# Kernel tuning notes

Measured on AMD Instinct MI355X. Metric: run time of the kernel, lower is better.

The kernel has to match this reference:

```python
import jax, jax.numpy as jnp
import numpy as np

B, S, D, H, M, K = 2048, 32, 1024, 1024, 4096, 32


def setup_inputs() -> dict:
    key = jax.random.key(0)
    ks = jax.random.split(key, 10)
    inp = {
        "x": jax.random.normal(ks[0], (B, S, D), dtype=jnp.float32),
        "topk": K,
        "W_enc": jax.random.normal(ks[1], (D, H), dtype=jnp.float32) * (1.0 / np.sqrt(D)),
        "b_enc": jnp.zeros((H,), dtype=jnp.float32),
        "w_curv": jax.random.normal(ks[2], (H, 1), dtype=jnp.float32) * (1.0 / np.sqrt(H)),
        "b_curv": jnp.zeros((1,), dtype=jnp.float32),
        "memory_slots": jax.random.normal(ks[3], (M, H), dtype=jnp.float32),
        "assoc": jax.random.normal(ks[4], (M, M), dtype=jnp.float32) * 0.01,
        "W_dec": jax.random.normal(ks[5], (H, D), dtype=jnp.float32) * (1.0 / np.sqrt(H)),
        "b_dec": jnp.zeros((D,), dtype=jnp.float32),
        "temperature": jnp.asarray(1.0, dtype=jnp.float32),
    }
    return inp


def reference(x, topk, W_enc, b_enc, w_curv, b_curv, memory_slots, assoc, W_dec, b_dec, temperature):
    # encoder + pooled query
    enc = jnp.tanh(x @ W_enc + b_enc)          # [B,S,H]
    query = enc.mean(axis=1)                   # [B,H]

    # content-based addressing (active_slots == M, temperature buffer)
    sim = jnp.einsum('bd,md->bm', query, memory_slots)        # [B,M]
    gate = jax.nn.sigmoid(query @ w_curv + b_curv)            # [B,1]
    sim = sim * (0.5 + gate) / jnp.maximum(temperature, 1e-6)
    vals, idx = jax.lax.top_k(sim, topk)                      # [B,K], sorted desc (matches torch.topk)

    # associative activation: two rounds of softmax -> assoc matmul
    act = jnp.einsum('bd,md->bm', query, memory_slots)        # [B,M]
    for _ in range(2):
        act = jax.nn.softmax(act, axis=-1) @ assoc

    # combine top-k scores with gathered associative activations
    comb = jax.nn.softmax(vals + jnp.take_along_axis(act, idx, axis=1), axis=-1)  # [B,K]
    mem = memory_slots[idx]                                   # [B,K,H] gather
    read = jnp.einsum('bk,bkh->bh', comb, mem)                # [B,H]

    out = jnp.tanh(read @ W_dec + b_dec)                      # [B,D]
    return jnp.broadcast_to(out[:, None, :], (x.shape[0], x.shape[1], out.shape[-1]))
```

## Files before the change

### kernel.cpp

```cpp
#include <hip/hip_runtime.h>

typedef _Float16 f16;
typedef f16 f16x8 __attribute__((ext_vector_type(8)));
typedef float f32x4 __attribute__((ext_vector_type(4)));

#define BD 2048
#define SD 32
#define DD 1024
#define HD 1024
#define MD 4096
#define KD 32

__global__ void k_pack_rows(const float* __restrict__ in, f16* __restrict__ hi,
                            f16* __restrict__ lo, int N, int K) {
  int t = blockIdx.x * 256 + threadIdx.x;
  int total = (N >> 4) * (K >> 5) * 64;
  if (t >= total) return;
  int l16 = t & 15, quad = (t >> 4) & 3;
  int x = t >> 6;
  int kch = K >> 5;
  int kc = x % kch, nt = x / kch;
  const float* src = in + (size_t)(nt * 16 + l16) * K + kc * 32 + quad * 8;
  float4 u0 = *(const float4*)src;
  float4 u1 = *(const float4*)(src + 4);
  float v[8] = {u0.x, u0.y, u0.z, u0.w, u1.x, u1.y, u1.z, u1.w};
  f16x8 h, l;
#pragma unroll
  for (int e = 0; e < 8; ++e) {
    h[e] = (f16)v[e];
    l[e] = (f16)(v[e] - (float)h[e]);
  }
  ((f16x8*)hi)[t] = h;
  if (lo) ((f16x8*)lo)[t] = l;
}

__global__ void k_pack_T(const float* __restrict__ in, f16* __restrict__ hi,
                         f16* __restrict__ lo, int N, int K) {
  int t = blockIdx.x * 256 + threadIdx.x;
  int total = (N >> 4) * (K >> 5) * 64;
  if (t >= total) return;
  int l16 = t & 15, quad = (t >> 4) & 3;
  int x = t >> 6;
  int kch = K >> 5;
  int kc = x % kch, nt = x / kch;
  int col = nt * 16 + l16;
  int krow = kc * 32 + quad * 8;
  f16x8 h, l;
#pragma unroll
  for (int e = 0; e < 8; ++e) {
    float v = in[(size_t)(krow + e) * N + col];
    f16 hh = (f16)v;
    h[e] = hh;
    l[e] = (f16)(v - (float)hh);
  }
  ((f16x8*)hi)[t] = h;
  if (lo) ((f16x8*)lo)[t] = l;
}

template <int SPLIT, int EPI>
__global__ __launch_bounds__(256) void k_gemm(const void* __restrict__ Ap,
                                              const f16* __restrict__ Bhi,
                                              const f16* __restrict__ Blo,
                                              float* __restrict__ C,
                                              const float* __restrict__ bias,
                                              int M, int N, int K) {
  __shared__ f16 As[128 * 32];
  __shared__ f16 Asl[SPLIT ? 128 * 32 : 8];
  const int n0 = blockIdx.x * 128, m0 = blockIdx.y * 128;
  const int t = threadIdx.x;
  const int lane = t & 63, w = t >> 6;
  const int wm = w >> 1, wn = w & 1;
  const int quad = lane >> 4, l16 = lane & 15;
  const int srow = t >> 2, sseg = t & 3;
  const int swf = (srow >> 1) & 3;
  const int rwf = (l16 >> 1) & 3;
  const int kch = K >> 5;

  f32x4 acc[4][4] = {};

  for (int kc32 = 0; kc32 < kch; ++kc32) {
    const int kc = kc32 << 5;
    f16x8 bh[4], bl[4];
#pragma unroll
    for (int j = 0; j < 4; ++j) {
      size_t fi = (((size_t)((n0 >> 4) + wn * 4 + j) * kch + kc32) << 6) + (quad << 4) + l16;
      bh[j] = ((const f16x8*)Bhi)[fi];
      if (SPLIT) bl[j] = ((const f16x8*)Blo)[fi];
    }
#pragma unroll
    for (int rep = 0; rep < 2; ++rep) {
      int row = srow + rep * 64;
      int slot = row * 32 + ((sseg ^ swf) << 3);
      if (SPLIT) {
        const float* g = (const float*)Ap + (size_t)(m0 + row) * K + kc + sseg * 8;
        float4 u0 = *(const float4*)g;
        float4 u1 = *(const float4*)(g + 4);
        float v[8] = {u0.x, u0.y, u0.z, u0.w, u1.x, u1.y, u1.z, u1.w};
        f16x8 h, l;
#pragma unroll
        for (int e = 0; e < 8; ++e) {
          h[e] = (f16)v[e];
          l[e] = (f16)(v[e] - (float)h[e]);
        }
        *(f16x8*)(As + slot) = h;
        *(f16x8*)(Asl + slot) = l;
      } else {
        const f16* g = (const f16*)Ap + (size_t)(m0 + row) * K + kc + sseg * 8;
        *(f16x8*)(As + slot) = *(const f16x8*)g;
      }
    }
    __syncthreads();
    f16x8 ah[4], al[4];
#pragma unroll
    for (int i = 0; i < 4; ++i) {
      int off = (wm * 64 + i * 16 + l16) * 32 + ((quad ^ rwf) << 3);
      ah[i] = *(const f16x8*)(As + off);
      if (SPLIT) al[i] = *(const f16x8*)(Asl + off);
    }
    if (SPLIT) {
#pragma unroll
      for (int i = 0; i < 4; ++i)
#pragma unroll
        for (int j = 0; j < 4; ++j) {
          acc[i][j] = __builtin_amdgcn_mfma_f32_16x16x32_f16(ah[i], bh[j], acc[i][j], 0, 0, 0);
          acc[i][j] = __builtin_amdgcn_mfma_f32_16x16x32_f16(ah[i], bl[j], acc[i][j], 0, 0, 0);
          acc[i][j] = __builtin_amdgcn_mfma_f32_16x16x32_f16(al[i], bh[j], acc[i][j], 0, 0, 0);
        }
    } else {
#pragma unroll
      for (int i = 0; i < 4; ++i)
#pragma unroll
        for (int j = 0; j < 4; ++j)
          acc[i][j] = __builtin_amdgcn_mfma_f32_16x16x32_f16(ah[i], bh[j], acc[i][j], 0, 0, 0);
    }
    __syncthreads();
  }

  if (EPI == 0) {
#pragma unroll
    for (int i = 0; i < 4; ++i) {
#pragma unroll
      for (int j = 0; j < 4; ++j) {
        int row = m0 + wm * 64 + i * 16 + quad * 4;
        int col = n0 + wn * 64 + j * 16 + l16;
        float* cp = C + (size_t)row * N + col;
#pragma unroll
        for (int r = 0; r < 4; ++r) cp[(size_t)r * N] = acc[i][j][r];
      }
    }
  } else if (EPI == 2) {
#pragma unroll
    for (int i = 0; i < 4; ++i) {
#pragma unroll
      for (int j = 0; j < 4; ++j) {
        int row = m0 + wm * 64 + i * 16 + quad * 4;
        int col = n0 + wn * 64 + j * 16 + l16;
        float bv = bias[col];
        float* cp = C + (size_t)row * N + col;
#pragma unroll
        for (int r = 0; r < 4; ++r) cp[(size_t)r * N] = tanhf(acc[i][j][r] + bv);
      }
    }
  } else if (EPI == 3) {
#pragma unroll
    for (int i = 0; i < 4; ++i) {
#pragma unroll
      for (int j = 0; j < 4; ++j) {
        int row = m0 + wm * 64 + i * 16 + quad * 4;
        int col = n0 + wn * 64 + j * 16 + l16;
        float bv = bias[col];
        float vv[4];
#pragma unroll
        for (int r = 0; r < 4; ++r) vv[r] = tanhf(acc[i][j][r] + bv);
        for (int s = 0; s < SD; ++s) {
          float* cp = C + ((size_t)row * SD + s) * N + col;
#pragma unroll
          for (int r = 0; r < 4; ++r) cp[(size_t)r * SD * N] = vv[r];
        }
      }
    }
  } else {
#pragma unroll
    for (int j = 0; j < 4; ++j) {
      int col = n0 + wn * 64 + j * 16 + l16;
      float bv = bias[col];
      float g0 = 0.f, g1 = 0.f;
#pragma unroll
      for (int i = 0; i < 4; ++i) {
        float s = 0.f;
#pragma unroll
        for (int r = 0; r < 4; ++r) s += tanhf(acc[i][j][r] + bv);
        if (i < 2) g0 += s; else g1 += s;
      }
      g0 += __shfl_xor(g0, 16); g0 += __shfl_xor(g0, 32);
      g1 += __shfl_xor(g1, 16); g1 += __shfl_xor(g1, 32);
      if (quad == 0) {
        int grp = (m0 + wm * 64) >> 5;
        C[(size_t)grp * N + col] = g0 * (1.0f / 32.0f);
        C[(size_t)(grp + 1) * N + col] = g1 * (1.0f / 32.0f);
      }
    }
  }
}

__global__ void k_gate(const float* __restrict__ query, const float* __restrict__ w_curv,
                       const float* __restrict__ b_curv, const float* __restrict__ temp,
                       float* __restrict__ scale) {
  int b = blockIdx.x, t = threadIdx.x;
  float s = 0.f;
  for (int h = t; h < HD; h += 256) s += query[(size_t)b * HD + h] * w_curv[h];
#pragma unroll
  for (int off = 32; off; off >>= 1) s += __shfl_xor(s, off);
  __shared__ float red[4];
  if ((t & 63) == 0) red[t >> 6] = s;
  __syncthreads();
  if (t == 0) {
    float tot = red[0] + red[1] + red[2] + red[3] + b_curv[0];
    float g = 1.f / (1.f + expf(-tot));
    scale[b] = (0.5f + g) / fmaxf(temp[0], 1e-6f);
  }
}

__global__ void k_topk(const float* __restrict__ sim, const float* __restrict__ scale,
                       int* __restrict__ idx, float* __restrict__ vals) {
  int b = blockIdx.x, t = threadIdx.x;
  __shared__ float sv[MD];
  __shared__ float rv[4];
  __shared__ int ri[4];
  for (int i = t; i < MD; i += 256) sv[i] = sim[(size_t)b * MD + i];
  __syncthreads();
  float sc = scale[b];
  for (int k = 0; k < KD; ++k) {
    float bv = -1e30f;
    int bi = 0x7fffffff;
    for (int i = t; i < MD; i += 256) {
      float v = sv[i];
      if (v > bv) { bv = v; bi = i; }
    }
#pragma unroll
    for (int off = 1; off < 64; off <<= 1) {
      float ov = __shfl_xor(bv, off);
      int oi = __shfl_xor(bi, off);
      if (ov > bv || (ov == bv && oi < bi)) { bv = ov; bi = oi; }
    }
    if ((t & 63) == 0) { rv[t >> 6] = bv; ri[t >> 6] = bi; }
    __syncthreads();
    if (t == 0) {
      float fv = rv[0];
      int fi = ri[0];
#pragma unroll
      for (int u = 1; u < 4; ++u)
        if (rv[u] > fv || (rv[u] == fv && ri[u] < fi)) { fv = rv[u]; fi = ri[u]; }
      idx[b * KD + k] = fi;
      vals[b * KD + k] = fv * sc;
      sv[fi] = -1e30f;
    }
    __syncthreads();
  }
}

__global__ void k_softmax(const float* __restrict__ in, f16* __restrict__ out, int C) {
  int b = blockIdx.x, t = threadIdx.x;
  const float* row = in + (size_t)b * C;
  __shared__ float red[4];
  float m = -1e30f;
  for (int i = t; i < C; i += 256) m = fmaxf(m, row[i]);
#pragma unroll
  for (int off = 32; off; off >>= 1) m = fmaxf(m, __shfl_xor(m, off));
  if ((t & 63) == 0) red[t >> 6] = m;
  __syncthreads();
  m = fmaxf(fmaxf(red[0], red[1]), fmaxf(red[2], red[3]));
  __syncthreads();
  float s = 0.f;
  for (int i = t; i < C; i += 256) s += expf(row[i] - m);
#pragma unroll
  for (int off = 32; off; off >>= 1) s += __shfl_xor(s, off);
  if ((t & 63) == 0) red[t >> 6] = s;
  __syncthreads();
  s = red[0] + red[1] + red[2] + red[3];
  float inv = 1.f / s;
  for (int i = t; i < C; i += 256) out[(size_t)b * C + i] = (f16)(expf(row[i] - m) * inv);
}

__global__ void k_combine(const float* __restrict__ vals, const int* __restrict__ idx,
                          const float* __restrict__ act, const float* __restrict__ mem,
                          f16* __restrict__ read_h) {
  int b = blockIdx.x, t = threadIdx.x;
  __shared__ float comb[KD];
  __shared__ int sidx[KD];
  if (t < KD) {
    int id = idx[b * KD + t];
    sidx[t] = id;
    float e = vals[b * KD + t] + act[(size_t)b * MD + id];
    float m = e;
#pragma unroll
    for (int off = 16; off; off >>= 1) m = fmaxf(m, __shfl_xor(m, off));
    float p = expf(e - m);
    float s = p;
#pragma unroll
    for (int off = 16; off; off >>= 1) s += __shfl_xor(s, off);
    comb[t] = p / s;
  }
  __syncthreads();
  for (int h = t; h < HD; h += 256) {
    float a = 0.f;
#pragma unroll
    for (int k = 0; k < KD; ++k) a += comb[k] * mem[(size_t)sidx[k] * HD + h];
    read_h[(size_t)b * HD + h] = (f16)a;
  }
}

extern "C" void kernel_launch(void* const* d_in, const int* in_sizes, int n_in,
                              void* d_out, int out_size, void* d_ws, size_t ws_size,
                              hipStream_t stream) {
  const float* x      = (const float*)d_in[0];
  const float* W_enc  = (const float*)d_in[2];
  const float* b_enc  = (const float*)d_in[3];
  const float* w_curv = (const float*)d_in[4];
  const float* b_curv = (const float*)d_in[5];
  const float* mem    = (const float*)d_in[6];
  const float* assoc  = (const float*)d_in[7];
  const float* W_dec  = (const float*)d_in[8];
  const float* b_dec  = (const float*)d_in[9];
  const float* temp   = (const float*)d_in[10];
  float* out = (float*)d_out;

  char* ws = (char*)d_ws;
  size_t off = 0;
  auto alloc = [&](size_t bytes) {
    void* p = ws + off;
    off += (bytes + 255) & ~(size_t)255;
    return p;
  };
  f16* Wt_hi   = (f16*)alloc((size_t)HD * DD * 2);
  f16* Wt_lo   = (f16*)alloc((size_t)HD * DD * 2);
  f16* ms_hi   = (f16*)alloc((size_t)MD * HD * 2);
  f16* ms_lo   = (f16*)alloc((size_t)MD * HD * 2);
  f16* as_pk   = (f16*)alloc((size_t)MD * MD * 2);
  f16* wd_pk   = (f16*)alloc((size_t)HD * DD * 2);
  float* query = (float*)alloc((size_t)BD * HD * 4);
  float* scale = (float*)alloc((size_t)BD * 4);
  float* sim   = (float*)alloc((size_t)BD * MD * 4);
  int* idx     = (int*)alloc((size_t)BD * KD * 4);
  float* vals  = (float*)alloc((size_t)BD * KD * 4);
  f16* p_h     = (f16*)alloc((size_t)BD * MD * 2);
  f16* read_h  = (f16*)alloc((size_t)BD * HD * 2);
  (void)ws_size; (void)in_sizes; (void)n_in; (void)out_size;

  dim3 b256(256);
  k_pack_T<<<dim3((HD / 16) * (DD / 32) * 64 / 256), b256, 0, stream>>>(W_enc, Wt_hi, Wt_lo, HD, DD);
  k_pack_rows<<<dim3((MD / 16) * (HD / 32) * 64 / 256), b256, 0, stream>>>(mem, ms_hi, ms_lo, MD, HD);
  k_pack_T<<<dim3((MD / 16) * (MD / 32) * 64 / 256), b256, 0, stream>>>(assoc, as_pk, nullptr, MD, MD);
  k_pack_T<<<dim3((DD / 16) * (HD / 32) * 64 / 256), b256, 0, stream>>>(W_dec, wd_pk, nullptr, DD, HD);
  k_gemm<1, 1><<<dim3(HD / 128, BD * SD / 128), b256, 0, stream>>>(
      x, Wt_hi, Wt_lo, query, b_enc, BD * SD, HD, DD);
  k_gate<<<dim3(BD), b256, 0, stream>>>(query, w_curv, b_curv, temp, scale);
  k_gemm<1, 0><<<dim3(MD / 128, BD / 128), b256, 0, stream>>>(
      query, ms_hi, ms_lo, sim, nullptr, BD, MD, HD);
  k_topk<<<dim3(BD), b256, 0, stream>>>(sim, scale, idx, vals);
  k_softmax<<<dim3(BD), b256, 0, stream>>>(sim, p_h, MD);
  k_gemm<0, 0><<<dim3(MD / 128, BD / 128), b256, 0, stream>>>(
      p_h, as_pk, nullptr, sim, nullptr, BD, MD, MD);
  k_softmax<<<dim3(BD), b256, 0, stream>>>(sim, p_h, MD);
  k_gemm<0, 0><<<dim3(MD / 128, BD / 128), b256, 0, stream>>>(
      p_h, as_pk, nullptr, sim, nullptr, BD, MD, MD);
  k_combine<<<dim3(BD), b256, 0, stream>>>(vals, idx, sim, mem, read_h);
  k_gemm<0, 3><<<dim3(DD / 128, BD / 128), b256, 0, stream>>>(
      read_h, wd_pk, nullptr, out, b_dec, BD, DD, HD);
}
```

Baseline: 1.500 ms.

## Add double-buffered 256x128 GEMM kernel with XCD-aware block mapping

Adds a new GEMM kernel that uses 512-thread blocks computing 256x128 tiles, double-buffers the A tile in shared memory with register prefetch of the next 64-wide K slab, and raises wave priority around the MFMA blocks. Block indices are remapped so that M tiles are grouped per XCD, which should improve L2 reuse of B. The encoder, similarity and both assoc GEMMs switch to it, and the decoder GEMM stays on the old kernel. The goal is to hide global-load latency and cut sync overhead. The cost is a larger LDS footprint (more so for the split-precision variant) and higher register pressure, which can lower occupancy.

```diff
diff --git a/kernel.cpp b/kernel.cpp
--- a/kernel.cpp
+++ b/kernel.cpp
@@ -55,6 +55,183 @@
   }
   ((f16x8*)hi)[t] = h;
   if (lo) ((f16x8*)lo)[t] = l;
+}
+
+__device__ __forceinline__ void cvt_split8(const float4& u0, const float4& u1,
+                                           f16x8& h, f16x8& l) {
+  float v[8] = {u0.x, u0.y, u0.z, u0.w, u1.x, u1.y, u1.z, u1.w};
+#pragma unroll
+  for (int e = 0; e < 8; ++e) {
+    f16 hh = (f16)v[e];
+    h[e] = hh;
+    l[e] = (f16)(v[e] - (float)hh);
+  }
+}
+
+template <int SPLIT, int EPI>
+__global__ __launch_bounds__(512, 2) void k_gemm2(const void* __restrict__ Ap,
+                                                  const f16* __restrict__ Bhi,
+                                                  const f16* __restrict__ Blo,
+                                                  float* __restrict__ C,
+                                                  const float* __restrict__ bias,
+                                                  int M, int N, int K) {
+  __shared__ f16 As[2 * 2 * 256 * 32];
+  __shared__ f16 Asl[SPLIT ? 2 * 2 * 256 * 32 : 8];
+
+  const int ntc = N >> 7;
+  const int sblk = blockIdx.x;
+  const int xcd = sblk & 7, q = sblk >> 3;
+  const int nt = q % ntc;
+  const int mt = xcd + ((q / ntc) << 3);
+  const int m0 = mt << 8, n0 = nt << 7;
+
+  const int t = threadIdx.x;
+  const int lane = t & 63, w = t >> 6;
+  const int wm = w >> 1, wn = w & 1;
+  const int quad = lane >> 4, l16 = lane & 15;
+  const int rwf = (l16 >> 1) & 3;
+  const int kch = K >> 5;
+  const int NT = K >> 6;
+
+  int goff[4], sslot[4];
+#pragma unroll
+  for (int r = 0; r < 4; ++r) {
+    int lin = r * 512 + t;
+    int kc = lin >> 10;
+    int row = (lin >> 2) & 255;
+    int seg = lin & 3;
+    goff[r] = (m0 + row) * K + kc * 32 + seg * 8;
+    sslot[r] = kc * 8192 + row * 32 + ((seg ^ ((row >> 1) & 3)) << 3);
+  }
+
+  f32x4 acc[4][4] = {};
+
+#pragma unroll
+  for (int r = 0; r < 4; ++r) {
+    if (SPLIT) {
+      const float* g = (const float*)Ap + (size_t)goff[r];
+      float4 u0 = *(const float4*)g;
+      float4 u1 = *(const float4*)(g + 4);
+      f16x8 h, l;
+      cvt_split8(u0, u1, h, l);
+      *(f16x8*)(As + sslot[r]) = h;
+      *(f16x8*)(Asl + sslot[r]) = l;
+    } else {
+      const f16* g = (const f16*)Ap + (size_t)goff[r];
+      *(f16x8*)(As + sslot[r]) = *(const f16x8*)g;
+    }
+  }
+  __syncthreads();
+
+  int cur = 0;
+  for (int kt = 0; kt < NT; ++kt) {
+    const bool pf = (kt + 1 < NT);
+    float4 nx0[4], nx1[4];
+    f16x8 nxh[4];
+    if (pf) {
+#pragma unroll
+      for (int r = 0; r < 4; ++r) {
+        if (SPLIT) {
+          const float* g = (const float*)Ap + (size_t)goff[r] + (size_t)(kt + 1) * 64;
+          nx0[r] = *(const float4*)g;
+          nx1[r] = *(const float4*)(g + 4);
+        } else {
+          const f16* g = (const f16*)Ap + (size_t)goff[r] + (size_t)(kt + 1) * 64;
+          nxh[r] = *(const f16x8*)g;
+        }
+      }
+    }
+    const f16* ba = As + cur * 16384;
+    const f16* bal = Asl + (SPLIT ? cur * 16384 : 0);
+#pragma unroll
+    for (int kc = 0; kc < 2; ++kc) {
+      const int kabs = kt * 2 + kc;
+      f16x8 bh[4], bl[4];
+#pragma unroll
+      for (int j = 0; j < 4; ++j) {
+        size_t fi = (((size_t)((n0 >> 4) + wn * 4 + j) * kch + kabs) << 6) + (quad << 4) + l16;
+        bh[j] = ((const f16x8*)Bhi)[fi];
+        if (SPLIT) bl[j] = ((const f16x8*)Blo)[fi];
+      }
+      f16x8 ah[4], al[4];
+#pragma unroll
+      for (int i = 0; i < 4; ++i) {
+        int off = kc * 8192 + (wm * 64 + i * 16 + l16) * 32 + ((quad ^ rwf) << 3);
+        ah[i] = *(const f16x8*)(ba + off);
+        if (SPLIT) al[i] = *(const f16x8*)(bal + off);
+      }
+      __builtin_amdgcn_s_setprio(1);
+      if (SPLIT) {
+#pragma unroll
+        for (int i = 0; i < 4; ++i)
+#pragma unroll
+          for (int j = 0; j < 4; ++j) {
+            acc[i][j] = __builtin_amdgcn_mfma_f32_16x16x32_f16(ah[i], bh[j], acc[i][j], 0, 0, 0);
+            acc[i][j] = __builtin_amdgcn_mfma_f32_16x16x32_f16(ah[i], bl[j], acc[i][j], 0, 0, 0);
+            acc[i][j] = __builtin_amdgcn_mfma_f32_16x16x32_f16(al[i], bh[j], acc[i][j], 0, 0, 0);
+          }
+      } else {
+#pragma unroll
+        for (int i = 0; i < 4; ++i)
+#pragma unroll
+          for (int j = 0; j < 4; ++j)
+            acc[i][j] = __builtin_amdgcn_mfma_f32_16x16x32_f16(ah[i], bh[j], acc[i][j], 0, 0, 0);
+      }
+      __builtin_amdgcn_s_setprio(0);
+    }
+    if (pf) {
+      f16* da = As + (cur ^ 1) * 16384;
+      f16* dal = Asl + (SPLIT ? (cur ^ 1) * 16384 : 0);
+#pragma unroll
+      for (int r = 0; r < 4; ++r) {
+        if (SPLIT) {
+          f16x8 h, l;
+          cvt_split8(nx0[r], nx1[r], h, l);
+          *(f16x8*)(da + sslot[r]) = h;
+          *(f16x8*)(dal + sslot[r]) = l;
+        } else {
+          *(f16x8*)(da + sslot[r]) = nxh[r];
+        }
+      }
+    }
+    __syncthreads();
+    cur ^= 1;
+  }
+
+  if (EPI == 0) {
+#pragma unroll
+    for (int i = 0; i < 4; ++i) {
+#pragma unroll
+      for (int j = 0; j < 4; ++j) {
+        int row = m0 + wm * 64 + i * 16 + quad * 4;
+        int col = n0 + wn * 64 + j * 16 + l16;
+        float* cp = C + (size_t)row * N + col;
+#pragma unroll
+        for (int r = 0; r < 4; ++r) cp[(size_t)r * N] = acc[i][j][r];
+      }
+    }
+  } else {
+#pragma unroll
+    for (int j = 0; j < 4; ++j) {
+      int col = n0 + wn * 64 + j * 16 + l16;
+      float bv = bias[col];
+      float g0 = 0.f, g1 = 0.f;
+#pragma unroll
+      for (int i = 0; i < 4; ++i) {
+        float s = 0.f;
+#pragma unroll
+        for (int r = 0; r < 4; ++r) s += tanhf(acc[i][j][r] + bv);
+        if (i < 2) g0 += s; else g1 += s;
+      }
+      g0 += __shfl_xor(g0, 16); g0 += __shfl_xor(g0, 32);
+      g1 += __shfl_xor(g1, 16); g1 += __shfl_xor(g1, 32);
+      if (quad == 0) {
+        int grp = (m0 + wm * 64) >> 5;
+        C[(size_t)grp * N + col] = g0 * (1.0f / 32.0f);
+        C[(size_t)(grp + 1) * N + col] = g1 * (1.0f / 32.0f);
+      }
+    }
+  }
 }
 
 template <int SPLIT, int EPI>
@@ -95,13 +272,8 @@
         const float* g = (const float*)Ap + (size_t)(m0 + row) * K + kc + sseg * 8;
         float4 u0 = *(const float4*)g;
         float4 u1 = *(const float4*)(g + 4);
-        float v[8] = {u0.x, u0.y, u0.z, u0.w, u1.x, u1.y, u1.z, u1.w};
         f16x8 h, l;
-#pragma unroll
-        for (int e = 0; e < 8; ++e) {
-          h[e] = (f16)v[e];
-          l[e] = (f16)(v[e] - (float)h[e]);
-        }
+        cvt_split8(u0, u1, h, l);
         *(f16x8*)(As + slot) = h;
         *(f16x8*)(Asl + slot) = l;
       } else {
@@ -347,22 +519,22 @@
   f16* read_h  = (f16*)alloc((size_t)BD * HD * 2);
   (void)ws_size; (void)in_sizes; (void)n_in; (void)out_size;
 
-  dim3 b256(256);
+  dim3 b256(256), b512(512);
   k_pack_T<<<dim3((HD / 16) * (DD / 32) * 64 / 256), b256, 0, stream>>>(W_enc, Wt_hi, Wt_lo, HD, DD);
   k_pack_rows<<<dim3((MD / 16) * (HD / 32) * 64 / 256), b256, 0, stream>>>(mem, ms_hi, ms_lo, MD, HD);
   k_pack_T<<<dim3((MD / 16) * (MD / 32) * 64 / 256), b256, 0, stream>>>(assoc, as_pk, nullptr, MD, MD);
   k_pack_T<<<dim3((DD / 16) * (HD / 32) * 64 / 256), b256, 0, stream>>>(W_dec, wd_pk, nullptr, DD, HD);
-  k_gemm<1, 1><<<dim3(HD / 128, BD * SD / 128), b256, 0, stream>>>(
+  k_gemm2<1, 1><<<dim3((BD * SD / 256) * (HD / 128)), b512, 0, stream>>>(
       x, Wt_hi, Wt_lo, query, b_enc, BD * SD, HD, DD);
   k_gate<<<dim3(BD), b256, 0, stream>>>(query, w_curv, b_curv, temp, scale);
-  k_gemm<1, 0><<<dim3(MD / 128, BD / 128), b256, 0, stream>>>(
+  k_gemm2<1, 0><<<dim3((BD / 256) * (MD / 128)), b512, 0, stream>>>(
       query, ms_hi, ms_lo, sim, nullptr, BD, MD, HD);
   k_topk<<<dim3(BD), b256, 0, stream>>>(sim, scale, idx, vals);
   k_softmax<<<dim3(BD), b256, 0, stream>>>(sim, p_h, MD);
-  k_gemm<0, 0><<<dim3(MD / 128, BD / 128), b256, 0, stream>>>(
+  k_gemm2<0, 0><<<dim3((BD / 256) * (MD / 128)), b512, 0, stream>>>(
       p_h, as_pk, nullptr, sim, nullptr, BD, MD, MD);
   k_softmax<<<dim3(BD), b256, 0, stream>>>(sim, p_h, MD);
-  k_gemm<0, 0><<<dim3(MD / 128, BD / 128), b256, 0, stream>>>(
+  k_gemm2<0, 0><<<dim3((BD / 256) * (MD / 128)), b512, 0, stream>>>(
       p_h, as_pk, nullptr, sim, nullptr, BD, MD, MD);
   k_combine<<<dim3(BD), b256, 0, stream>>>(vals, idx, sim, mem, read_h);
   k_gemm<0, 3><<<dim3(DD / 128, BD / 128), b256, 0, stream>>>(
```

After: 1.472 ms. Within noise of the previous version (-1.8%).
